# Kernel optimization log

Measured on AMD Instinct MI355X. Metric: run time of the kernel, lower is better.

Reference implementation:

```python
import jax, jax.numpy as jnp
import numpy as np

B, T, C, H = 2, 2048, 1024, 16
D = C // H  # head_dim = 64


def setup_inputs() -> dict:
    key = jax.random.key(0)
    k1, k2, k3, k4 = jax.random.split(key, 4)
    x = jax.random.normal(k1, (B, T, C), dtype=jnp.float32)
    # key_padding_mask: True for valid token, False for padding.
    # Use per-example valid lengths so the mask is realistic; every example
    # has length >= 1 so no softmax row is fully masked.
    lengths = jax.random.randint(k2, (B,), T // 2, T + 1)
    key_padding_mask = jnp.arange(T)[None, :] < lengths[:, None]
    Wqkv = jax.random.normal(k3, (3 * C, C), dtype=jnp.float32) * 0.02
    bqkv = jnp.zeros((3 * C,), dtype=jnp.float32)
    Wproj = jax.random.normal(k4, (C, C), dtype=jnp.float32) * 0.02
    bproj = jnp.zeros((C,), dtype=jnp.float32)
    return {"x": x, "key_padding_mask": key_padding_mask,
            "Wqkv": Wqkv, "bqkv": bqkv, "Wproj": Wproj, "bproj": bproj}


def reference(x, key_padding_mask, Wqkv, bqkv, Wproj, bproj):
    # qkv projection (torch Linear: y = x @ W^T + b)
    qkv = jnp.einsum('btc,oc->bto', x, Wqkv) + bqkv          # (B,T,3C)
    q, k, v = jnp.split(qkv, 3, axis=-1)
    q = q.reshape(B, T, H, D)
    k = k.reshape(B, T, H, D)
    v = v.reshape(B, T, H, D)
    scale = 1.0 / np.sqrt(D).astype(np.float32)
    scores = jnp.einsum('bqhd,bkhd->bhqk', q, k) * scale      # (B,H,T,T)
    causal = jnp.tril(jnp.ones((T, T), dtype=bool))           # (T,T)
    mask = causal[None, None, :, :] & key_padding_mask[:, None, None, :]
    scores = jnp.where(mask, scores, -jnp.inf)
    attn = jax.nn.softmax(scores, axis=-1)                    # dropout p=0.0
    out = jnp.einsum('bhqk,bkhd->bqhd', attn, v).reshape(B, T, C)
    out = jnp.einsum('btc,oc->bto', out, Wproj) + bproj
    return out
```

## Files before the change

### kernel.cpp

```cpp
#include <hip/hip_runtime.h>
#include <hip/hip_bf16.h>
#include <stdint.h>

#define B_ 2
#define T_ 2048
#define C_ 1024
#define H_ 16
#define D_ 64

typedef __attribute__((ext_vector_type(8))) short bf16x8;
typedef __attribute__((ext_vector_type(4))) float f32x4;

__device__ __forceinline__ unsigned short f2bf(float f) {
  union { float f; uint32_t u; } c; c.f = f;
  uint32_t r = c.u + 0x7FFFu + ((c.u >> 16) & 1u);
  return (unsigned short)(r >> 16);
}

__device__ __forceinline__ uint32_t pack_bf16x2(float lo, float hi) {
  uint32_t r;
  asm("v_cvt_pk_bf16_f32 %0, %1, %2" : "=v"(r) : "v"(lo), "v"(hi));
  return r;
}

__device__ __forceinline__ void gload_lds16(const unsigned short* g,
                                            unsigned short* l) {
  __builtin_amdgcn_global_load_lds(
      (const __attribute__((address_space(1))) void*)(g),
      (__attribute__((address_space(3))) void*)(l), 16, 0, 0);
}

__global__ void cvt_f32_bf16(const float* __restrict__ s,
                             unsigned short* __restrict__ d, int n4) {
  int i = blockIdx.x * blockDim.x + threadIdx.x;
  if (i >= n4) return;
  float4 v = ((const float4*)s)[i];
  ushort4 o;
  o.x = f2bf(v.x); o.y = f2bf(v.y); o.z = f2bf(v.z); o.w = f2bf(v.w);
  ((ushort4*)d)[i] = o;
}

__global__ void compute_lengths(const unsigned int* __restrict__ mask,
                                int* __restrict__ lens) {
  int lane = threadIdx.x;
  unsigned int w0 = mask[0];
  for (int b = 0; b < B_; ++b) {
    int cnt = 0;
    if (w0 == 1u) {
      for (int t = lane; t < T_; t += 64) cnt += (mask[(size_t)b * T_ + t] != 0u);
    } else if (w0 == 0x3F800000u) {
      const float* mf = (const float*)mask;
      for (int t = lane; t < T_; t += 64) cnt += (mf[(size_t)b * T_ + t] != 0.f);
    } else {
      const unsigned char* mb = (const unsigned char*)mask;
      for (int t = lane; t < T_; t += 64) cnt += (mb[(size_t)b * T_ + t] != 0);
    }
    for (int off = 32; off > 0; off >>= 1) cnt += __shfl_down(cnt, off);
    if (lane == 0) lens[b] = cnt;
  }
}

__global__ __launch_bounds__(256)
void gemm_bt(const unsigned short* __restrict__ A,
             const unsigned short* __restrict__ Bm,
             const float* __restrict__ bias,
             float* __restrict__ outF,
             unsigned short* __restrict__ Qw,
             unsigned short* __restrict__ Kw,
             unsigned short* __restrict__ Vw,
             int N, int K, int mode) {
  __shared__ unsigned short As[128 * 64];
  __shared__ unsigned short Bs[128 * 64];
  const int tid = threadIdx.x;
  const int lane = tid & 63;
  const int w = tid >> 6;
  const int wm = w >> 1, wn = w & 1;
  const int q4 = lane >> 4, l15 = lane & 15;
  const int bm = blockIdx.y * 128;
  const int bn = blockIdx.x * 128;

  f32x4 acc[4][4] = {};

  for (int kt = 0; kt < K; kt += 64) {
#pragma unroll
    for (int i = 0; i < 4; ++i) {
      int r0 = w * 32 + i * 8;
      int row = r0 + (lane >> 3);
      int kc = (lane & 7) ^ (row & 7);
      gload_lds16(A + (size_t)(bm + row) * K + kt + kc * 8, &As[r0 * 64]);
      gload_lds16(Bm + (size_t)(bn + row) * K + kt + kc * 8, &Bs[r0 * 64]);
    }
    __syncthreads();
#pragma unroll
    for (int kk = 0; kk < 2; ++kk) {
      bf16x8 af[4], bfv[4];
#pragma unroll
      for (int mi = 0; mi < 4; ++mi) {
        int row = wm * 64 + mi * 16 + l15;
        int pc = (kk * 4 + q4) ^ (row & 7);
        af[mi] = *(const bf16x8*)(As + (size_t)row * 64 + pc * 8);
      }
#pragma unroll
      for (int ni = 0; ni < 4; ++ni) {
        int row = wn * 64 + ni * 16 + l15;
        int pc = (kk * 4 + q4) ^ (row & 7);
        bfv[ni] = *(const bf16x8*)(Bs + (size_t)row * 64 + pc * 8);
      }
#pragma unroll
      for (int mi = 0; mi < 4; ++mi)
#pragma unroll
        for (int ni = 0; ni < 4; ++ni)
          acc[mi][ni] = __builtin_amdgcn_mfma_f32_16x16x32_bf16(
              af[mi], bfv[ni], acc[mi][ni], 0, 0, 0);
    }
    __syncthreads();
  }

#pragma unroll
  for (int mi = 0; mi < 4; ++mi) {
    const int row0 = bm + wm * 64 + mi * 16 + q4 * 4;
#pragma unroll
    for (int ni = 0; ni < 4; ++ni) {
      const int col = bn + wn * 64 + ni * 16 + l15;
      const float bv = bias[col];
#pragma unroll
      for (int r = 0; r < 4; ++r) {
        const int row = row0 + r;
        float v = acc[mi][ni][r] + bv;
        if (mode == 1) {
          outF[(size_t)row * N + col] = v;
        } else {
          int b = row >> 11, t = row & (T_ - 1);
          int which = col >> 10, c = col & (C_ - 1);
          int h = c >> 6, dd = c & (D_ - 1);
          unsigned short* dst = (which == 0) ? Qw : ((which == 1) ? Kw : Vw);
          if (which == 0) v *= 0.1803368801111243f;
          dst[(((size_t)(b * H_ + h) * T_) + t) * D_ + dd] = f2bf(v);
        }
      }
    }
  }
}

__global__ __launch_bounds__(256)
void transpose_v(const unsigned short* __restrict__ V,
                 unsigned short* __restrict__ Vt) {
  __shared__ unsigned short tile[64][65];
  int bh = blockIdx.y;
  int t0 = blockIdx.x * 64;
  int tid = threadIdx.x;
  int r = tid >> 2, c0 = (tid & 3) * 16;
  const uint4* s4 = (const uint4*)(V + ((size_t)bh * T_ + t0 + r) * D_ + c0);
  union { uint4 v; unsigned short u[8]; } ua, ub;
  ua.v = s4[0]; ub.v = s4[1];
#pragma unroll
  for (int j = 0; j < 8; ++j) {
    tile[r][c0 + j] = ua.u[j];
    tile[r][c0 + 8 + j] = ub.u[j];
  }
  __syncthreads();
  int dd = tid >> 2, tt0 = (tid & 3) * 16;
  union { uint4 v[2]; unsigned short u[16]; } ov;
#pragma unroll
  for (int j = 0; j < 16; ++j) ov.u[j] = tile[tt0 + j][dd];
  uint4* dptr = (uint4*)(Vt + ((size_t)bh * D_ + dd) * T_ + t0 + tt0);
  dptr[0] = ov.v[0];
  dptr[1] = ov.v[1];
}

__global__ __launch_bounds__(256)
void attn_fwd(const unsigned short* __restrict__ Qw,
              const unsigned short* __restrict__ Kw,
              const unsigned short* __restrict__ Vt,
              unsigned short* __restrict__ AO,
              const int* __restrict__ lens) {
  __shared__ unsigned short Ks[2][64 * 64];
  __shared__ unsigned short Vs[2][64 * 64];
  __shared__ unsigned short Pb[4][32 * 64];

  const int bh = blockIdx.y;
  const int b = bh >> 4;
  const int h = bh & 15;
  const int qt = gridDim.x - 1 - blockIdx.x;
  const int q0 = qt * 128;
  const int tid = threadIdx.x;
  const int lane = tid & 63;
  const int w = tid >> 6;
  const int q4 = lane >> 4, l15 = lane & 15;
  const int len = lens[b];

  const unsigned short* Qp = Qw + (size_t)bh * T_ * D_;
  const unsigned short* Kp = Kw + (size_t)bh * T_ * D_;
  const unsigned short* Vp = Vt + (size_t)bh * D_ * T_;
  unsigned short* Pw = &Pb[w][0];

  const int qw0 = q0 + w * 32;
  const int qwmax = qw0 + 31;

  bf16x8 qf[2][2];
#pragma unroll
  for (int mi = 0; mi < 2; ++mi)
#pragma unroll
    for (int kk = 0; kk < 2; ++kk)
      qf[mi][kk] = *(const bf16x8*)(Qp + (size_t)(qw0 + mi * 16 + l15) * D_ +
                                    kk * 32 + q4 * 8);

  f32x4 ot[2][4] = {};
  float m[2] = {-INFINITY, -INFINITY};
  float lsum[2] = {0.f, 0.f};

  int kcap = q0 + 127;
  if (kcap > len - 1) kcap = len - 1;
  const int nkt = kcap / 64 + 1;

  const int srow = lane >> 3;
  const int scc = lane & 7;

#pragma unroll
  for (int i = 0; i < 2; ++i) {
    int r0 = w * 16 + i * 8;
    int rk = r0 + srow;
    int kc = scc ^ (rk & 7);
    gload_lds16(Kp + (size_t)rk * D_ + kc * 8, &Ks[0][r0 * 64]);
    gload_lds16(Vp + (size_t)rk * T_ + kc * 8, &Vs[0][r0 * 64]);
  }
  __syncthreads();

  int cur = 0;
  for (int kt = 0; kt < nkt; ++kt) {
    const int kbase = kt * 64;
    if (kt + 1 < nkt) {
      const int kb2 = kbase + 64;
#pragma unroll
      for (int i = 0; i < 2; ++i) {
        int r0 = w * 16 + i * 8;
        int rk = r0 + srow;
        int kc = scc ^ (rk & 7);
        gload_lds16(Kp + (size_t)(kb2 + rk) * D_ + kc * 8, &Ks[cur ^ 1][r0 * 64]);
        gload_lds16(Vp + (size_t)rk * T_ + kb2 + kc * 8, &Vs[cur ^ 1][r0 * 64]);
      }
    }

    if (kbase <= qwmax) {
      bf16x8 kfr[4][2];
#pragma unroll
      for (int nt = 0; nt < 4; ++nt)
#pragma unroll
        for (int kk = 0; kk < 2; ++kk) {
          int row = nt * 16 + l15;
          int pc = (kk * 4 + q4) ^ (row & 7);
          kfr[nt][kk] = *(const bf16x8*)(&Ks[cur][row * 64 + pc * 8]);
        }
      f32x4 st[4][2];
#pragma unroll
      for (int nt = 0; nt < 4; ++nt)
#pragma unroll
        for (int mi = 0; mi < 2; ++mi) {
          f32x4 z = {};
          z = __builtin_amdgcn_mfma_f32_16x16x32_bf16(kfr[nt][0], qf[mi][0], z, 0, 0, 0);
          z = __builtin_amdgcn_mfma_f32_16x16x32_bf16(kfr[nt][1], qf[mi][1], z, 0, 0, 0);
          st[nt][mi] = z;
        }
      float pmax[2] = {-INFINITY, -INFINITY};
#pragma unroll
      for (int nt = 0; nt < 4; ++nt)
#pragma unroll
        for (int mi = 0; mi < 2; ++mi) {
          int qq = qw0 + mi * 16 + l15;
#pragma unroll
          for (int r = 0; r < 4; ++r) {
            int kpos = kbase + nt * 16 + q4 * 4 + r;
            bool ok = (kpos < len) && (kpos <= qq);
            float v = ok ? st[nt][mi][r] : -INFINITY;
            st[nt][mi][r] = v;
            pmax[mi] = fmaxf(pmax[mi], v);
          }
        }
#pragma unroll
      for (int mi = 0; mi < 2; ++mi) {
        float v = pmax[mi];
        v = fmaxf(v, __shfl_xor(v, 16));
        v = fmaxf(v, __shfl_xor(v, 32));
        pmax[mi] = v;
      }
#pragma unroll
      for (int mi = 0; mi < 2; ++mi) {
        if (!__all(pmax[mi] <= m[mi] + 8.f)) {
          float mn = fmaxf(m[mi], pmax[mi]);
          float sc = exp2f(m[mi] - mn);
          m[mi] = mn;
          lsum[mi] *= sc;
#pragma unroll
          for (int dt = 0; dt < 4; ++dt)
#pragma unroll
            for (int r = 0; r < 4; ++r) ot[mi][dt][r] *= sc;
        }
      }
      float psum[2] = {0.f, 0.f};
#pragma unroll
      for (int nt = 0; nt < 4; ++nt)
#pragma unroll
        for (int mi = 0; mi < 2; ++mi) {
          float p0 = exp2f(st[nt][mi][0] - m[mi]);
          float p1 = exp2f(st[nt][mi][1] - m[mi]);
          float p2 = exp2f(st[nt][mi][2] - m[mi]);
          float p3 = exp2f(st[nt][mi][3] - m[mi]);
          psum[mi] += (p0 + p1) + (p2 + p3);
          uint32_t w0 = pack_bf16x2(p0, p1);
          uint32_t w1 = pack_bf16x2(p2, p3);
          int row = mi * 16 + l15;
          int c = nt * 4 + q4;
          int phys = c ^ ((l15 & 7) << 1);
          uint2 pr; pr.x = w0; pr.y = w1;
          *(uint2*)(&Pw[row * 64 + phys * 4]) = pr;
        }
#pragma unroll
      for (int mi = 0; mi < 2; ++mi) {
        float v = psum[mi];
        v += __shfl_xor(v, 16);
        v += __shfl_xor(v, 32);
        lsum[mi] += v;
      }
      bf16x8 vfr[4][2];
#pragma unroll
      for (int dt = 0; dt < 4; ++dt)
#pragma unroll
        for (int kk = 0; kk < 2; ++kk) {
          int row = dt * 16 + l15;
          int pc = (kk * 4 + q4) ^ (row & 7);
          vfr[dt][kk] = *(const bf16x8*)(&Vs[cur][row * 64 + pc * 8]);
        }
      bf16x8 pt[2][2];
#pragma unroll
      for (int mi = 0; mi < 2; ++mi)
#pragma unroll
        for (int kk = 0; kk < 2; ++kk) {
          int row = mi * 16 + l15;
          int c0 = kk * 8 + q4 * 2;
          int phys = c0 ^ ((l15 & 7) << 1);
          pt[mi][kk] = *(const bf16x8*)(&Pw[row * 64 + phys * 4]);
        }
#pragma unroll
      for (int mi = 0; mi < 2; ++mi)
#pragma unroll
        for (int dt = 0; dt < 4; ++dt) {
          ot[mi][dt] = __builtin_amdgcn_mfma_f32_16x16x32_bf16(
              vfr[dt][0], pt[mi][0], ot[mi][dt], 0, 0, 0);
          ot[mi][dt] = __builtin_amdgcn_mfma_f32_16x16x32_bf16(
              vfr[dt][1], pt[mi][1], ot[mi][dt], 0, 0, 0);
        }
    }

    __syncthreads();
    cur ^= 1;
  }

#pragma unroll
  for (int mi = 0; mi < 2; ++mi) {
    float inv = 1.f / lsum[mi];
    int qq = qw0 + mi * 16 + l15;
#pragma unroll
    for (int dt = 0; dt < 4; ++dt) {
      uint2 pr;
      pr.x = pack_bf16x2(ot[mi][dt][0] * inv, ot[mi][dt][1] * inv);
      pr.y = pack_bf16x2(ot[mi][dt][2] * inv, ot[mi][dt][3] * inv);
      *(uint2*)(&AO[(size_t)(b * T_ + qq) * C_ + h * 64 + dt * 16 + q4 * 4]) = pr;
    }
  }
}

extern "C" void kernel_launch(void* const* d_in, const int* in_sizes, int n_in,
                              void* d_out, int out_size, void* d_ws, size_t ws_size,
                              hipStream_t stream) {
  const float* x = (const float*)d_in[0];
  const unsigned int* mask = (const unsigned int*)d_in[1];
  const float* Wqkv = (const float*)d_in[2];
  const float* bqkv = (const float*)d_in[3];
  const float* Wproj = (const float*)d_in[4];
  const float* bproj = (const float*)d_in[5];
  float* out = (float*)d_out;

  unsigned short* XB = (unsigned short*)d_ws;
  unsigned short* WQ = XB + 4194304;
  unsigned short* WP = WQ + 3145728;
  unsigned short* Qw = WP + 1048576;
  unsigned short* Kw = Qw + 4194304;
  unsigned short* Vw = Kw + 4194304;
  unsigned short* Vt = Vw + 4194304;
  unsigned short* AO = Vt + 4194304;
  int* lens = (int*)(AO + 4194304);

  cvt_f32_bf16<<<4096, 256, 0, stream>>>(x, XB, 1048576);
  cvt_f32_bf16<<<3072, 256, 0, stream>>>(Wqkv, WQ, 786432);
  cvt_f32_bf16<<<1024, 256, 0, stream>>>(Wproj, WP, 262144);
  compute_lengths<<<1, 64, 0, stream>>>(mask, lens);

  gemm_bt<<<dim3(3072 / 128, 4096 / 128), 256, 0, stream>>>(
      XB, WQ, bqkv, nullptr, Qw, Kw, Vw, 3072, 1024, 0);

  transpose_v<<<dim3(T_ / 64, B_ * H_), 256, 0, stream>>>(Vw, Vt);

  attn_fwd<<<dim3(T_ / 128, B_ * H_), 256, 0, stream>>>(Qw, Kw, Vt, AO, lens);

  gemm_bt<<<dim3(1024 / 128, 4096 / 128), 256, 0, stream>>>(
      AO, WP, bproj, out, nullptr, nullptr, nullptr, 1024, 1024, 1);
}
```

Before: 251.4 us.

## Use 8 waves of 16 query rows per attention block, skip masking on interior tiles

The attention kernel now launches 512 threads per block. Each of 8 wavefronts owns 16 query rows instead of 4 wavefronts owning 32, which halves per-wave register state and spreads the K/V tile staging across more waves. A fast path also skips the per-element causal and padding mask when a key tile lies entirely inside the valid region. In exchange, K/V fragments loaded from LDS are reused across fewer query rows, so LDS reads per MFMA rise, and more waves share each block barrier.

New measurement: 232.3 us. 1.08x faster.

```diff
diff --git a/kernel.cpp b/kernel.cpp
--- a/kernel.cpp
+++ b/kernel.cpp
@@ -168,7 +168,7 @@
   dptr[1] = ov.v[1];
 }
 
-__global__ __launch_bounds__(256)
+__global__ __launch_bounds__(512)
 void attn_fwd(const unsigned short* __restrict__ Qw,
               const unsigned short* __restrict__ Kw,
               const unsigned short* __restrict__ Vt,
@@ -176,7 +176,7 @@
               const int* __restrict__ lens) {
   __shared__ unsigned short Ks[2][64 * 64];
   __shared__ unsigned short Vs[2][64 * 64];
-  __shared__ unsigned short Pb[4][32 * 64];
+  __shared__ unsigned short Pb[8][16 * 64];
 
   const int bh = blockIdx.y;
   const int b = bh >> 4;
@@ -194,20 +194,17 @@
   const unsigned short* Vp = Vt + (size_t)bh * D_ * T_;
   unsigned short* Pw = &Pb[w][0];
 
-  const int qw0 = q0 + w * 32;
-  const int qwmax = qw0 + 31;
-
-  bf16x8 qf[2][2];
-#pragma unroll
-  for (int mi = 0; mi < 2; ++mi)
-#pragma unroll
-    for (int kk = 0; kk < 2; ++kk)
-      qf[mi][kk] = *(const bf16x8*)(Qp + (size_t)(qw0 + mi * 16 + l15) * D_ +
-                                    kk * 32 + q4 * 8);
-
-  f32x4 ot[2][4] = {};
-  float m[2] = {-INFINITY, -INFINITY};
-  float lsum[2] = {0.f, 0.f};
+  const int qw0 = q0 + w * 16;
+  const int qwmax = qw0 + 15;
+
+  bf16x8 qf[2];
+#pragma unroll
+  for (int kk = 0; kk < 2; ++kk)
+    qf[kk] = *(const bf16x8*)(Qp + (size_t)(qw0 + l15) * D_ + kk * 32 + q4 * 8);
+
+  f32x4 ot[4] = {};
+  float m = -INFINITY;
+  float lsum = 0.f;
 
   int kcap = q0 + 127;
   if (kcap > len - 1) kcap = len - 1;
@@ -215,15 +212,12 @@
 
   const int srow = lane >> 3;
   const int scc = lane & 7;
-
-#pragma unroll
-  for (int i = 0; i < 2; ++i) {
-    int r0 = w * 16 + i * 8;
-    int rk = r0 + srow;
-    int kc = scc ^ (rk & 7);
-    gload_lds16(Kp + (size_t)rk * D_ + kc * 8, &Ks[0][r0 * 64]);
-    gload_lds16(Vp + (size_t)rk * T_ + kc * 8, &Vs[0][r0 * 64]);
-  }
+  const int sr0 = w * 8;
+  const int rk = sr0 + srow;
+  const int skc = scc ^ (rk & 7);
+
+  gload_lds16(Kp + (size_t)rk * D_ + skc * 8, &Ks[0][sr0 * 64]);
+  gload_lds16(Vp + (size_t)rk * T_ + skc * 8, &Vs[0][sr0 * 64]);
   __syncthreads();
 
   int cur = 0;
@@ -231,139 +225,111 @@
     const int kbase = kt * 64;
     if (kt + 1 < nkt) {
       const int kb2 = kbase + 64;
-#pragma unroll
-      for (int i = 0; i < 2; ++i) {
-        int r0 = w * 16 + i * 8;
-        int rk = r0 + srow;
-        int kc = scc ^ (rk & 7);
-        gload_lds16(Kp + (size_t)(kb2 + rk) * D_ + kc * 8, &Ks[cur ^ 1][r0 * 64]);
-        gload_lds16(Vp + (size_t)rk * T_ + kb2 + kc * 8, &Vs[cur ^ 1][r0 * 64]);
-      }
+      gload_lds16(Kp + (size_t)(kb2 + rk) * D_ + skc * 8, &Ks[cur ^ 1][sr0 * 64]);
+      gload_lds16(Vp + (size_t)rk * T_ + kb2 + skc * 8, &Vs[cur ^ 1][sr0 * 64]);
     }
 
     if (kbase <= qwmax) {
-      bf16x8 kfr[4][2];
-#pragma unroll
-      for (int nt = 0; nt < 4; ++nt)
-#pragma unroll
-        for (int kk = 0; kk < 2; ++kk) {
+      f32x4 st[4];
+#pragma unroll
+      for (int nt = 0; nt < 4; ++nt) {
+        bf16x8 kfr0, kfr1;
+        {
           int row = nt * 16 + l15;
-          int pc = (kk * 4 + q4) ^ (row & 7);
-          kfr[nt][kk] = *(const bf16x8*)(&Ks[cur][row * 64 + pc * 8]);
+          int pc0 = q4 ^ (row & 7);
+          int pc1 = (4 + q4) ^ (row & 7);
+          kfr0 = *(const bf16x8*)(&Ks[cur][row * 64 + pc0 * 8]);
+          kfr1 = *(const bf16x8*)(&Ks[cur][row * 64 + pc1 * 8]);
         }
-      f32x4 st[4][2];
-#pragma unroll
-      for (int nt = 0; nt < 4; ++nt)
-#pragma unroll
-        for (int mi = 0; mi < 2; ++mi) {
-          f32x4 z = {};
-          z = __builtin_amdgcn_mfma_f32_16x16x32_bf16(kfr[nt][0], qf[mi][0], z, 0, 0, 0);
-          z = __builtin_amdgcn_mfma_f32_16x16x32_bf16(kfr[nt][1], qf[mi][1], z, 0, 0, 0);
-          st[nt][mi] = z;
-        }
-      float pmax[2] = {-INFINITY, -INFINITY};
-#pragma unroll
-      for (int nt = 0; nt < 4; ++nt)
-#pragma unroll
-        for (int mi = 0; mi < 2; ++mi) {
-          int qq = qw0 + mi * 16 + l15;
+        f32x4 z = {};
+        z = __builtin_amdgcn_mfma_f32_16x16x32_bf16(kfr0, qf[0], z, 0, 0, 0);
+        z = __builtin_amdgcn_mfma_f32_16x16x32_bf16(kfr1, qf[1], z, 0, 0, 0);
+        st[nt] = z;
+      }
+      const bool interior = (kbase + 63 <= qw0) && (kbase + 63 < len);
+      float pmax = -INFINITY;
+      if (interior) {
+#pragma unroll
+        for (int nt = 0; nt < 4; ++nt)
+#pragma unroll
+          for (int r = 0; r < 4; ++r) pmax = fmaxf(pmax, st[nt][r]);
+      } else {
+        const int qq = qw0 + l15;
+#pragma unroll
+        for (int nt = 0; nt < 4; ++nt)
 #pragma unroll
           for (int r = 0; r < 4; ++r) {
             int kpos = kbase + nt * 16 + q4 * 4 + r;
             bool ok = (kpos < len) && (kpos <= qq);
-            float v = ok ? st[nt][mi][r] : -INFINITY;
-            st[nt][mi][r] = v;
-            pmax[mi] = fmaxf(pmax[mi], v);
+            float v = ok ? st[nt][r] : -INFINITY;
+            st[nt][r] = v;
+            pmax = fmaxf(pmax, v);
           }
+      }
+      pmax = fmaxf(pmax, __shfl_xor(pmax, 16));
+      pmax = fmaxf(pmax, __shfl_xor(pmax, 32));
+      if (!__all(pmax <= m + 8.f)) {
+        float mn = fmaxf(m, pmax);
+        float sc = exp2f(m - mn);
+        m = mn;
+        lsum *= sc;
+#pragma unroll
+        for (int dt = 0; dt < 4; ++dt)
+#pragma unroll
+          for (int r = 0; r < 4; ++r) ot[dt][r] *= sc;
+      }
+      float psum = 0.f;
+#pragma unroll
+      for (int nt = 0; nt < 4; ++nt) {
+        float p0 = exp2f(st[nt][0] - m);
+        float p1 = exp2f(st[nt][1] - m);
+        float p2 = exp2f(st[nt][2] - m);
+        float p3 = exp2f(st[nt][3] - m);
+        psum += (p0 + p1) + (p2 + p3);
+        uint32_t w0 = pack_bf16x2(p0, p1);
+        uint32_t w1 = pack_bf16x2(p2, p3);
+        int c = nt * 4 + q4;
+        int phys = c ^ ((l15 & 7) << 1);
+        uint2 pr; pr.x = w0; pr.y = w1;
+        *(uint2*)(&Pw[l15 * 64 + phys * 4]) = pr;
+      }
+      psum += __shfl_xor(psum, 16);
+      psum += __shfl_xor(psum, 32);
+      lsum += psum;
+      bf16x8 pt[2];
+#pragma unroll
+      for (int kk = 0; kk < 2; ++kk) {
+        int c0 = kk * 8 + q4 * 2;
+        int phys = c0 ^ ((l15 & 7) << 1);
+        pt[kk] = *(const bf16x8*)(&Pw[l15 * 64 + phys * 4]);
+      }
+#pragma unroll
+      for (int dt = 0; dt < 4; ++dt) {
+        bf16x8 vfr0, vfr1;
+        {
+          int row = dt * 16 + l15;
+          int pc0 = q4 ^ (row & 7);
+          int pc1 = (4 + q4) ^ (row & 7);
+          vfr0 = *(const bf16x8*)(&Vs[cur][row * 64 + pc0 * 8]);
+          vfr1 = *(const bf16x8*)(&Vs[cur][row * 64 + pc1 * 8]);
         }
-#pragma unroll
-      for (int mi = 0; mi < 2; ++mi) {
-        float v = pmax[mi];
-        v = fmaxf(v, __shfl_xor(v, 16));
-        v = fmaxf(v, __shfl_xor(v, 32));
-        pmax[mi] = v;
-      }
-#pragma unroll
-      for (int mi = 0; mi < 2; ++mi) {
-        if (!__all(pmax[mi] <= m[mi] + 8.f)) {
-          float mn = fmaxf(m[mi], pmax[mi]);
-          float sc = exp2f(m[mi] - mn);
-          m[mi] = mn;
-          lsum[mi] *= sc;
-#pragma unroll
-          for (int dt = 0; dt < 4; ++dt)
-#pragma unroll
-            for (int r = 0; r < 4; ++r) ot[mi][dt][r] *= sc;
-        }
-      }
-      float psum[2] = {0.f, 0.f};
-#pragma unroll
-      for (int nt = 0; nt < 4; ++nt)
-#pragma unroll
-        for (int mi = 0; mi < 2; ++mi) {
-          float p0 = exp2f(st[nt][mi][0] - m[mi]);
-          float p1 = exp2f(st[nt][mi][1] - m[mi]);
-          float p2 = exp2f(st[nt][mi][2] - m[mi]);
-          float p3 = exp2f(st[nt][mi][3] - m[mi]);
-          psum[mi] += (p0 + p1) + (p2 + p3);
-          uint32_t w0 = pack_bf16x2(p0, p1);
-          uint32_t w1 = pack_bf16x2(p2, p3);
-          int row = mi * 16 + l15;
-          int c = nt * 4 + q4;
-          int phys = c ^ ((l15 & 7) << 1);
-          uint2 pr; pr.x = w0; pr.y = w1;
-          *(uint2*)(&Pw[row * 64 + phys * 4]) = pr;
-        }
-#pragma unroll
-      for (int mi = 0; mi < 2; ++mi) {
-        float v = psum[mi];
-        v += __shfl_xor(v, 16);
-        v += __shfl_xor(v, 32);
-        lsum[mi] += v;
-      }
-      bf16x8 vfr[4][2];
-#pragma unroll
-      for (int dt = 0; dt < 4; ++dt)
-#pragma unroll
-        for (int kk = 0; kk < 2; ++kk) {
-          int row = dt * 16 + l15;
-          int pc = (kk * 4 + q4) ^ (row & 7);
-          vfr[dt][kk] = *(const bf16x8*)(&Vs[cur][row * 64 + pc * 8]);
-        }
-      bf16x8 pt[2][2];
-#pragma unroll
-      for (int mi = 0; mi < 2; ++mi)
-#pragma unroll
-        for (int kk = 0; kk < 2; ++kk) {
-          int row = mi * 16 + l15;
-          int c0 = kk * 8 + q4 * 2;
-          int phys = c0 ^ ((l15 & 7) << 1);
-          pt[mi][kk] = *(const bf16x8*)(&Pw[row * 64 + phys * 4]);
-        }
-#pragma unroll
-      for (int mi = 0; mi < 2; ++mi)
-#pragma unroll
-        for (int dt = 0; dt < 4; ++dt) {
-          ot[mi][dt] = __builtin_amdgcn_mfma_f32_16x16x32_bf16(
-              vfr[dt][0], pt[mi][0], ot[mi][dt], 0, 0, 0);
-          ot[mi][dt] = __builtin_amdgcn_mfma_f32_16x16x32_bf16(
-              vfr[dt][1], pt[mi][1], ot[mi][dt], 0, 0, 0);
-        }
+        ot[dt] = __builtin_amdgcn_mfma_f32_16x16x32_bf16(vfr0, pt[0], ot[dt], 0, 0, 0);
+        ot[dt] = __builtin_amdgcn_mfma_f32_16x16x32_bf16(vfr1, pt[1], ot[dt], 0, 0, 0);
+      }
     }
 
     __syncthreads();
     cur ^= 1;
   }
 
-#pragma unroll
-  for (int mi = 0; mi < 2; ++mi) {
-    float inv = 1.f / lsum[mi];
-    int qq = qw0 + mi * 16 + l15;
+  {
+    float inv = 1.f / lsum;
+    int qq = qw0 + l15;
 #pragma unroll
     for (int dt = 0; dt < 4; ++dt) {
       uint2 pr;
-      pr.x = pack_bf16x2(ot[mi][dt][0] * inv, ot[mi][dt][1] * inv);
-      pr.y = pack_bf16x2(ot[mi][dt][2] * inv, ot[mi][dt][3] * inv);
+      pr.x = pack_bf16x2(ot[dt][0] * inv, ot[dt][1] * inv);
+      pr.y = pack_bf16x2(ot[dt][2] * inv, ot[dt][3] * inv);
       *(uint2*)(&AO[(size_t)(b * T_ + qq) * C_ + h * 64 + dt * 16 + q4 * 4]) = pr;
     }
   }
@@ -400,7 +366,7 @@
 
   transpose_v<<<dim3(T_ / 64, B_ * H_), 256, 0, stream>>>(Vw, Vt);
 
-  attn_fwd<<<dim3(T_ / 128, B_ * H_), 256, 0, stream>>>(Qw, Kw, Vt, AO, lens);
+  attn_fwd<<<dim3(T_ / 128, B_ * H_), 512, 0, stream>>>(Qw, Kw, Vt, AO, lens);
 
   gemm_bt<<<dim3(1024 / 128, 4096 / 128), 256, 0, stream>>>(
       AO, WP, bproj, out, nullptr, nullptr, nullptr, 1024, 1024, 1);
```
